# Performance work log

Measured on AMD Instinct MI355X. Metric: run time of the kernel, lower is better.

The kernel has to match this reference:

```python
import jax, jax.numpy as jnp
import numpy as np
from math import comb

LEVEL = 16
LENGTH = 64
TOPK = 2
SIZE = 512
BATCH = 32
NEG = -1e8


def _catalan(n_leaves):
    # number of distinct binary trees over n_leaves leaves
    m = n_leaves - 1
    return comb(2 * m, m) // (m + 1)


def _offsets(length, level):
    # cell offset of each chart level: level l occupies (length - l) cells
    return np.cumsum([0] + [length - l for l in range(level)])


def setup_inputs() -> dict:
    key = jax.random.key(0)
    K, B, size, level, length = TOPK, BATCH, SIZE, LEVEL, LENGTH
    L, N = length - level, level
    off = _offsets(length, level)
    ncells = int(off[-1])
    ks = jax.random.split(key, 5)
    chart_h = jax.random.normal(ks[0], (K, B, ncells, size), jnp.float32)
    chart_s = jax.random.normal(ks[1], (K, B, ncells, 1), jnp.float32)
    mat = jax.random.normal(ks[2], (size, size), jnp.float32) / np.sqrt(size).astype(np.float32)
    Wc = jax.random.normal(ks[3], (2 * size, size), jnp.float32) / np.sqrt(2 * size).astype(np.float32)
    bc = jnp.zeros((size,), jnp.float32)
    # structural gather indices: left child = (level n, pos), right child = (level level-1-n, pos+n+1)
    l_idx = np.zeros((L, N), np.int64)
    r_idx = np.zeros((L, N), np.int64)
    for pos in range(L):
        for n in range(N):
            l_idx[pos, n] = off[n] + pos
            r_idx[pos, n] = off[level - 1 - n] + pos + n + 1
    return {
        'chart_h': chart_h, 'chart_s': chart_s,
        'l_index': jnp.asarray(l_idx.reshape(-1)), 'r_index': jnp.asarray(r_idx.reshape(-1)),
        'mat': mat, 'Wc': Wc, 'bc': bc,
    }


def _penalty_mask(level, N, K):
    # Faithful to penalize_incomplete_splits: idx = i // K**2 == 0 for i < K*K,
    # so only the n_idx==0 block is ever penalized. l_level=0, r_level=level-1.
    M = N * K * K
    mask = np.zeros(M, bool)
    for i in range(K * K):
        lk, rk = i // K, i % K
        if _catalan(0 + 1) < lk + 1 or _catalan((level - 1) + 1) < rk + 1:
            mask[i] = True
    return jnp.asarray(mask)


def reference(chart_h, chart_s, l_index, r_index, mat, Wc, bc):
    K, B, ncells, size = chart_h.shape
    level = LEVEL
    N = level
    L = l_index.shape[0] // N
    M = N * K * K
    # gather child states from charts: (K,B,L,N,size) -> (B,L,N,K,size)
    lh = jnp.moveaxis(chart_h[:, :, l_index].reshape(K, B, L, N, size), 0, 3)
    rh = jnp.moveaxis(chart_h[:, :, r_index].reshape(K, B, L, N, size), 0, 3)
    ls = jnp.moveaxis(chart_s[:, :, l_index].reshape(K, B, L, N), 0, 3)  # (B,L,N,K)
    rs = jnp.moveaxis(chart_s[:, :, r_index].reshape(K, B, L, N), 0, 3)
    # bilinear composition score: (B,L,N,K_l,K_r)
    s_raw = jnp.einsum('blnkd,de,blnje->blnkj', lh, mat, rh)
    # flat combo index = n*K*K + lk*K + rk; add child scores
    s = (s_raw + ls[..., :, None] + rs[..., None, :]).reshape(B, L, M)
    s = jnp.where(_penalty_mask(level, N, K), jnp.float32(NEG), s)
    topk_s, topk_idx = jax.lax.top_k(s, K)  # (B,L,K), sorted descending like torch.topk
    # dense compose over all N*K*K combos
    combo_lh = jnp.repeat(lh, K, axis=3).reshape(B, L, M, size)   # lk = z // K
    combo_rh = jnp.tile(rh, (1, 1, 1, K, 1)).reshape(B, L, M, size)  # rk = z % K
    all_h = jnp.tanh(jnp.concatenate([combo_lh, combo_rh], axis=-1) @ Wc + bc)
    topk_h = jnp.take_along_axis(all_h, topk_idx[..., None], axis=2)  # (B,L,K,size)
    # UnitNorm normalize_func
    topk_h = topk_h / jnp.linalg.norm(topk_h, axis=-1, keepdims=True)
    topk_s = topk_s[..., None]  # (B,L,K,1) to match torch shape
    if _catalan(N + 1) < K:  # static no-op at this level
        topk_s = topk_s.at[:, :, _catalan(N + 1):].set(NEG)
    topk_n_idx = topk_idx // (K * K)
    topk_lk = (topk_idx % (K * K)) // K
    topk_rk = (topk_idx % (K * K)) % K
    return topk_h, topk_s, topk_n_idx, topk_lk, topk_rk
```

## Files before the change

kernel.cpp:

```cpp
#include <hip/hip_runtime.h>
#include <cstdint>
#include <cstddef>

#define B_DIM   32
#define L_DIM   48
#define NCELLS  904
#define SZ      512
#define NEGF    (-1e8f)
#define DELTA   0.25f
#define MAXC    32

#define OFF_S   1572864
#define OFF_N   1575936
#define OFF_L   1579008
#define OFF_R   1582080

typedef _Float16  f16x8 __attribute__((ext_vector_type(8)));
typedef float     f32x4 __attribute__((ext_vector_type(4)));

static __device__ __forceinline__ uint16_t f2bf(float f) {
    uint32_t u = __builtin_bit_cast(uint32_t, f);
    u += 0x7fffu + ((u >> 16) & 1u);
    return (uint16_t)(u >> 16);
}

#define GLD16(gp, lp) __builtin_amdgcn_global_load_lds(                        \
        (__attribute__((address_space(1))) void*)(gp),                         \
        (__attribute__((address_space(3))) void*)(lp), 16, 0, 0)

static __device__ __forceinline__ int level_off(int n) {
    return n * 64 - (n * (n - 1)) / 2;
}

__global__ __launch_bounds__(256)
void prep_mat(const float* __restrict__ mat, _Float16* __restrict__ P)
{
    const int tg   = blockIdx.x * 256 + threadIdx.x;
    const int c    = tg >> 6, lane = tg & 63;
    const int srow = 16 * (c & 31) + (lane & 15);
    const int scol = 32 * (c >> 5) + (lane >> 4) * 8;
    const float4 a = *(const float4*)(mat + (size_t)srow * 512 + scol);
    const float4 b = *(const float4*)(mat + (size_t)srow * 512 + scol + 4);
    f16x8 w;
    w[0]=(_Float16)(a.x*64.f); w[1]=(_Float16)(a.y*64.f);
    w[2]=(_Float16)(a.z*64.f); w[3]=(_Float16)(a.w*64.f);
    w[4]=(_Float16)(b.x*64.f); w[5]=(_Float16)(b.y*64.f);
    w[6]=(_Float16)(b.z*64.f); w[7]=(_Float16)(b.w*64.f);
    *(f16x8*)(P + (size_t)tg * 8) = w;
}

__global__ __launch_bounds__(256)
void conv_h(const float* __restrict__ x, _Float16* __restrict__ y)
{
    const size_t i = ((size_t)blockIdx.x * 256 + threadIdx.x) * 8;
    const float4 a = *(const float4*)(x + i);
    const float4 b = *(const float4*)(x + i + 4);
    f16x8 w;
    w[0]=(_Float16)(a.x*16.f); w[1]=(_Float16)(a.y*16.f);
    w[2]=(_Float16)(a.z*16.f); w[3]=(_Float16)(a.w*16.f);
    w[4]=(_Float16)(b.x*16.f); w[5]=(_Float16)(b.y*16.f);
    w[6]=(_Float16)(b.z*16.f); w[7]=(_Float16)(b.w*16.f);
    *(f16x8*)(y + i) = w;
}

__global__ __launch_bounds__(256, 2)
void gemm_fused(const _Float16* __restrict__ A16,
                const _Float16* __restrict__ P,
                _Float16* __restrict__ C)
{
    __shared__ _Float16 As16[64 * 512];

    const int t = threadIdx.x;
    const int wave = t >> 6, lane = t & 63;
    const int n0 = blockIdx.x * 256;
    const int nq = n0 >> 4;
    const int m0 = blockIdx.y * 64;
    const int col_l = lane & 15, quad = lane >> 4;

#pragma unroll
    for (int i = 0; i < 16; ++i) {
        const int r = wave * 16 + i;
        GLD16(A16 + (size_t)(m0 + r) * 512 + ((lane ^ (r & 7)) * 8),
              (char*)As16 + r * 1024);
    }
    __syncthreads();

    f32x4 acc[4][4];
#pragma unroll
    for (int i = 0; i < 4; ++i)
#pragma unroll
        for (int j = 0; j < 4; ++j) acc[i][j] = (f32x4){0.f, 0.f, 0.f, 0.f};

#pragma unroll 4
    for (int w16 = 0; w16 < 16; ++w16) {
        f16x8 af[4];
#pragma unroll
        for (int mi = 0; mi < 4; ++mi) {
            const int r = mi * 16 + col_l;
            const int u = w16 * 4 + quad;
            af[mi] = *(const f16x8*)&As16[r * 512 + (u ^ (r & 7)) * 8];
        }
#pragma unroll
        for (int ni = 0; ni < 4; ++ni) {
            const int c = w16 * 32 + nq + wave * 4 + ni;
            const f16x8 bf = *(const f16x8*)(P + (size_t)c * 512 + lane * 8);
#pragma unroll
            for (int mi = 0; mi < 4; ++mi)
                acc[mi][ni] = __builtin_amdgcn_mfma_f32_16x16x32_f16(
                    af[mi], bf, acc[mi][ni], 0, 0, 0);
        }
    }

#pragma unroll
    for (int ni = 0; ni < 4; ++ni) {
        const int ncol = n0 + wave * 64 + ni * 16 + col_l;
#pragma unroll
        for (int mi = 0; mi < 4; ++mi) {
            const int mrow = m0 + mi * 16 + quad * 4;
#pragma unroll
            for (int r = 0; r < 4; ++r)
                C[(size_t)(mrow + r) * 512 + ncol] = (_Float16)acc[mi][ni][r];
        }
    }
}

static __device__ __forceinline__ void emit_outputs(
    int row, int i1, int i2, float v1, float v2, float* out)
{
    out[OFF_S + row * 2 + 0] = v1;
    out[OFF_S + row * 2 + 1] = v2;
    out[OFF_N + row * 2 + 0] = (float)(i1 >> 2);
    out[OFF_N + row * 2 + 1] = (float)(i2 >> 2);
    out[OFF_L + row * 2 + 0] = (float)((i1 >> 1) & 1);
    out[OFF_L + row * 2 + 1] = (float)((i2 >> 1) & 1);
    out[OFF_R + row * 2 + 0] = (float)(i1 & 1);
    out[OFF_R + row * 2 + 1] = (float)(i2 & 1);
}

static __device__ __forceinline__ void gather_x(
    int row, int pos, int b, const int* top_z,
    const float* __restrict__ chart_h, uint16_t* __restrict__ X, int tid)
{
#pragma unroll
    for (int kq = 0; kq < 2; ++kq) {
        const int z = top_z[kq];
        const int n = z >> 2, lk = (z >> 1) & 1, rk = z & 1;
        const int lcell = level_off(n) + pos;
        const int rcell = level_off(15 - n) + pos + n + 1;
        const float* srcl = chart_h + ((size_t)(lk * B_DIM + b) * NCELLS + lcell) * SZ;
        const float* srcr = chart_h + ((size_t)(rk * B_DIM + b) * NCELLS + rcell) * SZ;
        uint16_t* dst = X + ((size_t)row * 2 + kq) * 1024;
        const int e = tid * 2;
        const float2 a = *(const float2*)(srcl + e);
        const float2 c = *(const float2*)(srcr + e);
        *(uint32_t*)(dst + e)       = (uint32_t)f2bf(a.x) | ((uint32_t)f2bf(a.y) << 16);
        *(uint32_t*)(dst + 512 + e) = (uint32_t)f2bf(c.x) | ((uint32_t)f2bf(c.y) << 16);
    }
}

__global__ __launch_bounds__(256)
void score_topk(const float* __restrict__ chart_h,
                const _Float16* __restrict__ CH16,
                const _Float16* __restrict__ T16,
                const float* __restrict__ chart_s,
                uint32_t* __restrict__ items,
                int* __restrict__ rowbase,
                int* __restrict__ counter,
                int* __restrict__ flags,
                uint16_t* __restrict__ X,
                float* __restrict__ out)
{
    const int b   = blockIdx.x / L_DIM;
    const int pos = blockIdx.x % L_DIM;
    const int row = blockIdx.x;
    const int wave = threadIdx.x >> 6, lane = threadIdx.x & 63;

    __shared__ float s_sh[64];
    __shared__ int top_z[2];
    __shared__ int flag_sh;

#pragma unroll
    for (int ni = 0; ni < 4; ++ni) {
        const int n = wave * 4 + ni;
        const int lcell = level_off(n) + pos;
        const int rcell = level_off(15 - n) + pos + n + 1;

        const f16x8 lv0 = *(const f16x8*)(CH16 + ((size_t)(0 * B_DIM + b) * NCELLS + lcell) * SZ + lane * 8);
        const f16x8 lv1 = *(const f16x8*)(CH16 + ((size_t)(1 * B_DIM + b) * NCELLS + lcell) * SZ + lane * 8);
        const f16x8 t0 = *(const f16x8*)(T16 + ((size_t)(0 * B_DIM + b) * NCELLS + rcell) * SZ + lane * 8);
        const f16x8 t1 = *(const f16x8*)(T16 + ((size_t)(1 * B_DIM + b) * NCELLS + rcell) * SZ + lane * 8);

        float d00 = 0.f, d01 = 0.f, d10 = 0.f, d11 = 0.f;
#pragma unroll
        for (int j = 0; j < 8; ++j) {
            const float c0 = (float)t0[j], c1 = (float)t1[j];
            const float l0 = (float)lv0[j], l1 = (float)lv1[j];
            d00 += l0 * c0; d01 += l0 * c1;
            d10 += l1 * c0; d11 += l1 * c1;
        }
#pragma unroll
        for (int o = 32; o > 0; o >>= 1) {
            d00 += __shfl_down(d00, o);
            d01 += __shfl_down(d01, o);
            d10 += __shfl_down(d10, o);
            d11 += __shfl_down(d11, o);
        }
        if (lane == 0) {
            const float ls0 = chart_s[(size_t)(0 * B_DIM + b) * NCELLS + lcell];
            const float ls1 = chart_s[(size_t)(1 * B_DIM + b) * NCELLS + lcell];
            const float rs0 = chart_s[(size_t)(0 * B_DIM + b) * NCELLS + rcell];
            const float rs1 = chart_s[(size_t)(1 * B_DIM + b) * NCELLS + rcell];
            const float inv = 1.0f / 16384.0f;
            s_sh[n * 4 + 0] = d00 * inv + ls0 + rs0;
            s_sh[n * 4 + 1] = d01 * inv + ls0 + rs1;
            s_sh[n * 4 + 2] = d10 * inv + ls1 + rs0;
            s_sh[n * 4 + 3] = d11 * inv + ls1 + rs1;
        }
    }
    __syncthreads();

    if (threadIdx.x < 64) {
        float v = s_sh[lane];
        if (lane == 2 || lane == 3) v = NEGF;
        float v1 = v; int i1 = lane;
#pragma unroll
        for (int o = 32; o > 0; o >>= 1) {
            float ov = __shfl_down(v1, o);
            int   oi = __shfl_down(i1, o);
            if (ov > v1 || (ov == v1 && oi < i1)) { v1 = ov; i1 = oi; }
        }
        v1 = __shfl(v1, 0); i1 = __shfl(i1, 0);
        float v2 = (lane == i1) ? -3.4e38f : v; int i2 = lane;
#pragma unroll
        for (int o = 32; o > 0; o >>= 1) {
            float ov = __shfl_down(v2, o);
            int   oi = __shfl_down(i2, o);
            if (ov > v2 || (ov == v2 && oi < i2)) { v2 = ov; i2 = oi; }
        }
        v2 = __shfl(v2, 0); i2 = __shfl(i2, 0);
        float v3 = (lane == i1 || lane == i2) ? -3.4e38f : v;
#pragma unroll
        for (int o = 32; o > 0; o >>= 1) {
            const float ov = __shfl_down(v3, o);
            if (ov > v3) v3 = ov;
        }
        v3 = __shfl(v3, 0);

        const int f = (v1 - v2 < DELTA) || (v2 - v3 < DELTA);
        const bool cand = (v >= v2 - DELTA);
        const unsigned long long mask = __ballot(cand);
        const int nc_full = __popcll(mask);
        const int nc = nc_full < MAXC ? nc_full : MAXC;
        int base = 0;
        if (lane == 0) {
            flags[row] = f ? nc : 0;
            flag_sh = f;
            if (f) base = atomicAdd(counter, nc);
            rowbase[row] = base;
            top_z[0] = i1; top_z[1] = i2;
            if (!f) emit_outputs(row, i1, i2, v1, v2, out);
        }
        base = __shfl(base, 0);
        if (f && cand) {
            const int rank = __popcll(mask & ((1ull << lane) - 1ull));
            if (rank < MAXC) items[base + rank] = ((uint32_t)row << 6) | (uint32_t)lane;
        }
    }
    __syncthreads();

    if (!flag_sh)
        gather_x(row, pos, b, top_z, chart_h, X, threadIdx.x);
}

__global__ __launch_bounds__(256)
void refine_eval(const float* __restrict__ chart_h,
                 const float* __restrict__ chart_s,
                 const float* __restrict__ mat,
                 const uint32_t* __restrict__ items,
                 const int* __restrict__ counter,
                 float* __restrict__ exval)
{
    const int total = *counter;
    const int t = threadIdx.x;
    const int wave = t >> 6, lane = t & 63;

    __shared__ float lh_sh[2][512];
    __shared__ float psum[2][4];

    for (int p = blockIdx.x; 2 * p < total; p += gridDim.x) {
        const int it0 = 2 * p;
        const int it1v = (2 * p + 1 < total);
        const uint32_t item0 = items[it0];
        const uint32_t item1 = it1v ? items[it0 + 1] : item0;

        int rowA = item0 >> 6, zA = item0 & 63;
        int bA = rowA / L_DIM, posA = rowA % L_DIM;
        int nA = zA >> 2, lkA = (zA >> 1) & 1, rkA = zA & 1;
        int lcA = level_off(nA) + posA, rcA = level_off(15 - nA) + posA + nA + 1;
        int rowB = item1 >> 6, zB = item1 & 63;
        int bB = rowB / L_DIM, posB = rowB % L_DIM;
        int nB = zB >> 2, lkB = (zB >> 1) & 1, rkB = zB & 1;
        int lcB = level_off(nB) + posB, rcB = level_off(15 - nB) + posB + nB + 1;

        const float* lhA = chart_h + ((size_t)(lkA * B_DIM + bA) * NCELLS + lcA) * SZ;
        const float* rhA = chart_h + ((size_t)(rkA * B_DIM + bA) * NCELLS + rcA) * SZ;
        const float* lhB = chart_h + ((size_t)(lkB * B_DIM + bB) * NCELLS + lcB) * SZ;
        const float* rhB = chart_h + ((size_t)(rkB * B_DIM + bB) * NCELLS + rcB) * SZ;

        __syncthreads();
        lh_sh[0][t] = lhA[t]; lh_sh[0][t + 256] = lhA[t + 256];
        lh_sh[1][t] = lhB[t]; lh_sh[1][t + 256] = lhB[t + 256];
        const float4 rA0 = *(const float4*)(rhA + lane * 8);
        const float4 rA1 = *(const float4*)(rhA + lane * 8 + 4);
        const float4 rB0 = *(const float4*)(rhB + lane * 8);
        const float4 rB1 = *(const float4*)(rhB + lane * 8 + 4);
        __syncthreads();

        const float* mb = mat + (size_t)(wave * 128) * 512 + lane * 8;
        float a00 = 0.f, a01 = 0.f, b00 = 0.f, b01 = 0.f;
        for (int e = 0; e < 128; e += 2) {
            const float4 m0 = *(const float4*)(mb + (size_t)(e + 0) * 512);
            const float4 m1 = *(const float4*)(mb + (size_t)(e + 0) * 512 + 4);
            const float4 m2 = *(const float4*)(mb + (size_t)(e + 1) * 512);
            const float4 m3 = *(const float4*)(mb + (size_t)(e + 1) * 512 + 4);
            const int eg = wave * 128 + e;
            const float lA0 = lh_sh[0][eg],     lB0 = lh_sh[1][eg];
            const float lA1 = lh_sh[0][eg + 1], lB1 = lh_sh[1][eg + 1];
            const float dA0 = m0.x*rA0.x + m0.y*rA0.y + m0.z*rA0.z + m0.w*rA0.w
                            + m1.x*rA1.x + m1.y*rA1.y + m1.z*rA1.z + m1.w*rA1.w;
            const float dB0 = m0.x*rB0.x + m0.y*rB0.y + m0.z*rB0.z + m0.w*rB0.w
                            + m1.x*rB1.x + m1.y*rB1.y + m1.z*rB1.z + m1.w*rB1.w;
            const float dA1 = m2.x*rA0.x + m2.y*rA0.y + m2.z*rA0.z + m2.w*rA0.w
                            + m3.x*rA1.x + m3.y*rA1.y + m3.z*rA1.z + m3.w*rA1.w;
            const float dB1 = m2.x*rB0.x + m2.y*rB0.y + m2.z*rB0.z + m2.w*rB0.w
                            + m3.x*rB1.x + m3.y*rB1.y + m3.z*rB1.z + m3.w*rB1.w;
            a00 += lA0 * dA0; a01 += lA1 * dA1;
            b00 += lB0 * dB0; b01 += lB1 * dB1;
        }
        float sA = a00 + a01, sB = b00 + b01;
#pragma unroll
        for (int o = 32; o > 0; o >>= 1) {
            sA += __shfl_down(sA, o);
            sB += __shfl_down(sB, o);
        }
        if (lane == 0) { psum[0][wave] = sA; psum[1][wave] = sB; }
        __syncthreads();
        if (t == 0) {
            const float lsA = chart_s[(size_t)(lkA * B_DIM + bA) * NCELLS + lcA];
            const float rsA = chart_s[(size_t)(rkA * B_DIM + bA) * NCELLS + rcA];
            exval[it0] = psum[0][0] + psum[0][1] + psum[0][2] + psum[0][3] + lsA + rsA;
            if (it1v) {
                const float lsB = chart_s[(size_t)(lkB * B_DIM + bB) * NCELLS + lcB];
                const float rsB = chart_s[(size_t)(rkB * B_DIM + bB) * NCELLS + rcB];
                exval[it0 + 1] = psum[1][0] + psum[1][1] + psum[1][2] + psum[1][3] + lsB + rsB;
            }
        }
    }
}

__global__ __launch_bounds__(256)
void refine_pick(const float* __restrict__ chart_h,
                 const uint32_t* __restrict__ items,
                 const int* __restrict__ rowbase,
                 const int* __restrict__ flags,
                 const float* __restrict__ exval,
                 uint16_t* __restrict__ X,
                 float* __restrict__ out)
{
    const int row = blockIdx.x;
    const int nc = flags[row];
    if (nc == 0) return;
    const int b = row / L_DIM, pos = row % L_DIM;
    const int t = threadIdx.x;

    __shared__ int top_z[2];

    if (t == 0) {
        const int base = rowbase[row];
        float v1 = -3.4e38f; int c1 = -1;
        for (int c = 0; c < nc; ++c) {
            const float v = exval[base + c];
            if (v > v1) { v1 = v; c1 = c; }
        }
        float v2 = -3.4e38f; int c2 = -1;
        for (int c = 0; c < nc; ++c) {
            if (c == c1) continue;
            const float v = exval[base + c];
            if (v > v2) { v2 = v; c2 = c; }
        }
        const int i1 = (int)(items[base + c1] & 63u);
        const int i2 = (int)(items[base + c2] & 63u);
        top_z[0] = i1; top_z[1] = i2;
        emit_outputs(row, i1, i2, v1, v2, out);
    }
    __syncthreads();
    gather_x(row, pos, b, top_z, chart_h, X, t);
}

__global__ __launch_bounds__(256)
void transpose_wc(const float* __restrict__ Wc, uint16_t* __restrict__ WcT)
{
    __shared__ float tbuf[64][65];
    const int i0 = blockIdx.x * 64;
    const int o0 = blockIdx.y * 64;
    const int c = threadIdx.x & 63, r4 = threadIdx.x >> 6;
    for (int rr = r4; rr < 64; rr += 4)
        tbuf[rr][c] = Wc[(size_t)(i0 + rr) * 512 + o0 + c];
    __syncthreads();
    for (int rr = r4; rr < 64; rr += 4)
        WcT[(size_t)(o0 + rr) * 1024 + i0 + c] = f2bf(tbuf[c][rr]);
}

typedef __bf16 bf16x8 __attribute__((ext_vector_type(8)));

__global__ __launch_bounds__(256, 2)
void gemm_compose(const uint16_t* __restrict__ A,
                  const uint16_t* __restrict__ Bm,
                  const float* __restrict__ bias,
                  float* __restrict__ C,
                  int M, int Nn, int Kk)
{
    __shared__ uint16_t As[128 * 64];
    __shared__ uint16_t Bs[128 * 64];

    const int tid  = threadIdx.x;
    const int wave = tid >> 6, lane = tid & 63;
    const int m0 = blockIdx.x * 128, n0 = blockIdx.y * 128;
    const int wm = (wave & 1) * 64, wn = (wave >> 1) * 64;
    const int col_l = lane & 15, quad = lane >> 4;
    const int lrow = lane >> 3;
    const int lcol = (lane & 7) * 8;

    f32x4 acc[4][4];
#pragma unroll
    for (int i = 0; i < 4; ++i)
#pragma unroll
        for (int j = 0; j < 4; ++j) acc[i][j] = (f32x4){0.f, 0.f, 0.f, 0.f};

    for (int k0 = 0; k0 < Kk; k0 += 64) {
        __syncthreads();
#pragma unroll
        for (int i = 0; i < 4; ++i) {
            const int q = wave * 4 + i;
            const int r = q * 8 + lrow;
            GLD16(A  + (size_t)(m0 + r) * Kk + k0 + lcol, (char*)As + q * 1024);
            GLD16(Bm + (size_t)(n0 + r) * Kk + k0 + lcol, (char*)Bs + q * 1024);
        }
        __syncthreads();
#pragma unroll
        for (int kk = 0; kk < 64; kk += 32) {
            bf16x8 af[4], bfr[4];
#pragma unroll
            for (int mi = 0; mi < 4; ++mi)
                af[mi] = *(const bf16x8*)&As[(wm + mi * 16 + col_l) * 64 + kk + quad * 8];
#pragma unroll
            for (int ni = 0; ni < 4; ++ni)
                bfr[ni] = *(const bf16x8*)&Bs[(wn + ni * 16 + col_l) * 64 + kk + quad * 8];
#pragma unroll
            for (int mi = 0; mi < 4; ++mi)
#pragma unroll
                for (int ni = 0; ni < 4; ++ni)
                    acc[mi][ni] = __builtin_amdgcn_mfma_f32_16x16x32_bf16(
                        af[mi], bfr[ni], acc[mi][ni], 0, 0, 0);
        }
    }

#pragma unroll
    for (int ni = 0; ni < 4; ++ni) {
        const int ncol = n0 + wn + ni * 16 + col_l;
        const float bv = bias[ncol];
#pragma unroll
        for (int mi = 0; mi < 4; ++mi) {
            const int mrow = m0 + wm + mi * 16 + quad * 4;
#pragma unroll
            for (int r = 0; r < 4; ++r)
                C[(size_t)(mrow + r) * Nn + ncol] = tanhf(acc[mi][ni][r] + bv);
        }
    }
}

__global__ __launch_bounds__(256)
void norm_rows(const float* __restrict__ H, float* __restrict__ out)
{
    const int row = blockIdx.x;
    const float* h = H + (size_t)row * SZ;
    const int t = threadIdx.x;
    const int wave = t >> 6, lane = t & 63;
    const float a = h[t], c = h[t + 256];
    float ss = a * a + c * c;
#pragma unroll
    for (int o = 32; o > 0; o >>= 1) ss += __shfl_down(ss, o);
    __shared__ float wsum[4];
    if (lane == 0) wsum[wave] = ss;
    __syncthreads();
    const float inv = rsqrtf(wsum[0] + wsum[1] + wsum[2] + wsum[3]);
    out[(size_t)row * SZ + t]       = a * inv;
    out[(size_t)row * SZ + t + 256] = c * inv;
}

extern "C" void kernel_launch(void* const* d_in, const int* in_sizes, int n_in,
                              void* d_out, int out_size, void* d_ws, size_t ws_size,
                              hipStream_t stream)
{
    const float* chart_h = (const float*)d_in[0];
    const float* chart_s = (const float*)d_in[1];
    const float* mat = (const float*)d_in[4];
    const float* Wc  = (const float*)d_in[5];
    const float* bc  = (const float*)d_in[6];
    float* out = (float*)d_out;

    char* ws = (char*)d_ws;
    _Float16* T16   = (_Float16*)ws;
    _Float16* MAT16 = (_Float16*)(ws + 59244544);
    uint32_t* ITEMS = (uint32_t*)(ws + 59768832);
    float*    EXVAL = (float*)(ws + 59965440);
    int*      RBASE = (int*)(ws + 60162048);
    int*      CNT   = (int*)(ws + 60168192);
    int*      FLAGS = (int*)(ws + 60168448);
    uint16_t* X     = (uint16_t*)(ws + 60174592);
    _Float16* CH16  = (_Float16*)(ws + 66466048);
    uint16_t* WcT   = (uint16_t*)ws;
    float*    H     = (float*)(ws + 1048576);

    hipMemsetAsync(CNT, 0, 4, stream);
    prep_mat<<<dim3(128), 256, 0, stream>>>(mat, MAT16);
    conv_h<<<dim3(14464), 256, 0, stream>>>(chart_h, CH16);
    gemm_fused<<<dim3(2, 904), 256, 0, stream>>>(CH16, MAT16, T16);
    score_topk<<<dim3(B_DIM * L_DIM), 256, 0, stream>>>(chart_h, CH16, T16, chart_s,
                                                        ITEMS, RBASE, CNT, FLAGS, X, out);
    transpose_wc<<<dim3(16, 8), 256, 0, stream>>>(Wc, WcT);
    refine_eval<<<dim3(1024), 256, 0, stream>>>(chart_h, chart_s, mat, ITEMS, CNT, EXVAL);
    refine_pick<<<dim3(B_DIM * L_DIM), 256, 0, stream>>>(chart_h, ITEMS, RBASE, FLAGS,
                                                         EXVAL, X, out);
    gemm_compose<<<dim3(24, 4), 256, 0, stream>>>(X, WcT, bc, H, 3072, 512, 1024);
    norm_rows<<<dim3(3072), 256, 0, stream>>>(H, out);
}
```

Baseline: 341.6 us.

## Fuse mat-projection GEMM into score kernel, computing only needed right-child rows

The standalone GEMM that projected every chart cell through mat and wrote a large fp16 T buffer to global memory is removed. Each score block now loads its 32 right-child rows (16 splits × 2 k) into shared memory, multiplies them by the fp16 mat with MFMA, and keeps the result in shared memory for the dot products. This removes the round trip of the T buffer through global memory and skips projecting cells that are never used as right children. In exchange, every block rereads the whole fp16 mat from cache and needs more shared memory per block. conv_h also now converts 16 elements per thread, and the workspace layout is compacted so CH16 and WcT share space.

```diff
diff --git a/kernel.cpp b/kernel.cpp
--- a/kernel.cpp
+++ b/kernel.cpp
@@ -52,75 +52,17 @@
 __global__ __launch_bounds__(256)
 void conv_h(const float* __restrict__ x, _Float16* __restrict__ y)
 {
-    const size_t i = ((size_t)blockIdx.x * 256 + threadIdx.x) * 8;
-    const float4 a = *(const float4*)(x + i);
-    const float4 b = *(const float4*)(x + i + 4);
-    f16x8 w;
-    w[0]=(_Float16)(a.x*16.f); w[1]=(_Float16)(a.y*16.f);
-    w[2]=(_Float16)(a.z*16.f); w[3]=(_Float16)(a.w*16.f);
-    w[4]=(_Float16)(b.x*16.f); w[5]=(_Float16)(b.y*16.f);
-    w[6]=(_Float16)(b.z*16.f); w[7]=(_Float16)(b.w*16.f);
-    *(f16x8*)(y + i) = w;
-}
-
-__global__ __launch_bounds__(256, 2)
-void gemm_fused(const _Float16* __restrict__ A16,
-                const _Float16* __restrict__ P,
-                _Float16* __restrict__ C)
-{
-    __shared__ _Float16 As16[64 * 512];
-
-    const int t = threadIdx.x;
-    const int wave = t >> 6, lane = t & 63;
-    const int n0 = blockIdx.x * 256;
-    const int nq = n0 >> 4;
-    const int m0 = blockIdx.y * 64;
-    const int col_l = lane & 15, quad = lane >> 4;
-
-#pragma unroll
-    for (int i = 0; i < 16; ++i) {
-        const int r = wave * 16 + i;
-        GLD16(A16 + (size_t)(m0 + r) * 512 + ((lane ^ (r & 7)) * 8),
-              (char*)As16 + r * 1024);
-    }
-    __syncthreads();
-
-    f32x4 acc[4][4];
-#pragma unroll
-    for (int i = 0; i < 4; ++i)
-#pragma unroll
-        for (int j = 0; j < 4; ++j) acc[i][j] = (f32x4){0.f, 0.f, 0.f, 0.f};
-
-#pragma unroll 4
-    for (int w16 = 0; w16 < 16; ++w16) {
-        f16x8 af[4];
-#pragma unroll
-        for (int mi = 0; mi < 4; ++mi) {
-            const int r = mi * 16 + col_l;
-            const int u = w16 * 4 + quad;
-            af[mi] = *(const f16x8*)&As16[r * 512 + (u ^ (r & 7)) * 8];
-        }
-#pragma unroll
-        for (int ni = 0; ni < 4; ++ni) {
-            const int c = w16 * 32 + nq + wave * 4 + ni;
-            const f16x8 bf = *(const f16x8*)(P + (size_t)c * 512 + lane * 8);
-#pragma unroll
-            for (int mi = 0; mi < 4; ++mi)
-                acc[mi][ni] = __builtin_amdgcn_mfma_f32_16x16x32_f16(
-                    af[mi], bf, acc[mi][ni], 0, 0, 0);
-        }
-    }
-
-#pragma unroll
-    for (int ni = 0; ni < 4; ++ni) {
-        const int ncol = n0 + wave * 64 + ni * 16 + col_l;
-#pragma unroll
-        for (int mi = 0; mi < 4; ++mi) {
-            const int mrow = m0 + mi * 16 + quad * 4;
-#pragma unroll
-            for (int r = 0; r < 4; ++r)
-                C[(size_t)(mrow + r) * 512 + ncol] = (_Float16)acc[mi][ni][r];
-        }
+    const size_t i = ((size_t)blockIdx.x * 256 + threadIdx.x) * 16;
+#pragma unroll
+    for (int h = 0; h < 2; ++h) {
+        const float4 a = *(const float4*)(x + i + h * 8);
+        const float4 b = *(const float4*)(x + i + h * 8 + 4);
+        f16x8 w;
+        w[0]=(_Float16)(a.x*16.f); w[1]=(_Float16)(a.y*16.f);
+        w[2]=(_Float16)(a.z*16.f); w[3]=(_Float16)(a.w*16.f);
+        w[4]=(_Float16)(b.x*16.f); w[5]=(_Float16)(b.y*16.f);
+        w[6]=(_Float16)(b.z*16.f); w[7]=(_Float16)(b.w*16.f);
+        *(f16x8*)(y + i + h * 8) = w;
     }
 }
 
@@ -158,26 +100,77 @@
     }
 }
 
-__global__ __launch_bounds__(256)
-void score_topk(const float* __restrict__ chart_h,
-                const _Float16* __restrict__ CH16,
-                const _Float16* __restrict__ T16,
-                const float* __restrict__ chart_s,
-                uint32_t* __restrict__ items,
-                int* __restrict__ rowbase,
-                int* __restrict__ counter,
-                int* __restrict__ flags,
-                uint16_t* __restrict__ X,
-                float* __restrict__ out)
-{
-    const int b   = blockIdx.x / L_DIM;
-    const int pos = blockIdx.x % L_DIM;
-    const int row = blockIdx.x;
-    const int wave = threadIdx.x >> 6, lane = threadIdx.x & 63;
-
+__global__ __launch_bounds__(256, 2)
+void score_fused(const float* __restrict__ chart_h,
+                 const _Float16* __restrict__ CH16,
+                 const _Float16* __restrict__ P,
+                 const float* __restrict__ chart_s,
+                 uint32_t* __restrict__ items,
+                 int* __restrict__ rowbase,
+                 int* __restrict__ counter,
+                 int* __restrict__ flags,
+                 uint16_t* __restrict__ X,
+                 float* __restrict__ out)
+{
+    __shared__ _Float16 Arh[32 * 512];
+    __shared__ _Float16 Ts[32 * 512];
     __shared__ float s_sh[64];
     __shared__ int top_z[2];
     __shared__ int flag_sh;
+
+    const int row = blockIdx.x;
+    const int b   = row / L_DIM;
+    const int pos = row % L_DIM;
+    const int t = threadIdx.x;
+    const int wave = t >> 6, lane = t & 63;
+    const int col_l = lane & 15, quad = lane >> 4;
+
+#pragma unroll
+    for (int i = 0; i < 8; ++i) {
+        const int r = wave * 8 + i;
+        const int k = r >> 4, n = r & 15;
+        const int rcell = level_off(15 - n) + pos + n + 1;
+        const size_t grow = (size_t)(k * B_DIM + b) * NCELLS + rcell;
+        GLD16(CH16 + grow * 512 + ((lane ^ (r & 7)) * 8),
+              (char*)Arh + r * 1024);
+    }
+    __syncthreads();
+
+    f32x4 acc[2][8];
+#pragma unroll
+    for (int i = 0; i < 2; ++i)
+#pragma unroll
+        for (int j = 0; j < 8; ++j) acc[i][j] = (f32x4){0.f, 0.f, 0.f, 0.f};
+
+#pragma unroll 4
+    for (int w16 = 0; w16 < 16; ++w16) {
+        f16x8 af[2];
+#pragma unroll
+        for (int mi = 0; mi < 2; ++mi) {
+            const int r = mi * 16 + col_l;
+            const int u = w16 * 4 + quad;
+            af[mi] = *(const f16x8*)&Arh[r * 512 + (u ^ (r & 7)) * 8];
+        }
+#pragma unroll
+        for (int ni = 0; ni < 8; ++ni) {
+            const int c = w16 * 32 + wave * 8 + ni;
+            const f16x8 bf = *(const f16x8*)(P + (size_t)c * 512 + lane * 8);
+#pragma unroll
+            for (int mi = 0; mi < 2; ++mi)
+                acc[mi][ni] = __builtin_amdgcn_mfma_f32_16x16x32_f16(
+                    af[mi], bf, acc[mi][ni], 0, 0, 0);
+        }
+    }
+
+#pragma unroll
+    for (int mi = 0; mi < 2; ++mi)
+#pragma unroll
+        for (int ni = 0; ni < 8; ++ni)
+#pragma unroll
+            for (int rr = 0; rr < 4; ++rr)
+                Ts[(mi * 16 + quad * 4 + rr) * 512 + wave * 128 + ni * 16 + col_l]
+                    = (_Float16)acc[mi][ni][rr];
+    __syncthreads();
 
 #pragma unroll
     for (int ni = 0; ni < 4; ++ni) {
@@ -187,8 +180,8 @@
 
         const f16x8 lv0 = *(const f16x8*)(CH16 + ((size_t)(0 * B_DIM + b) * NCELLS + lcell) * SZ + lane * 8);
         const f16x8 lv1 = *(const f16x8*)(CH16 + ((size_t)(1 * B_DIM + b) * NCELLS + lcell) * SZ + lane * 8);
-        const f16x8 t0 = *(const f16x8*)(T16 + ((size_t)(0 * B_DIM + b) * NCELLS + rcell) * SZ + lane * 8);
-        const f16x8 t1 = *(const f16x8*)(T16 + ((size_t)(1 * B_DIM + b) * NCELLS + rcell) * SZ + lane * 8);
+        const f16x8 t0 = *(const f16x8*)&Ts[(0 * 16 + n) * 512 + lane * 8];
+        const f16x8 t1 = *(const f16x8*)&Ts[(1 * 16 + n) * 512 + lane * 8];
 
         float d00 = 0.f, d01 = 0.f, d10 = 0.f, d11 = 0.f;
 #pragma unroll
@@ -510,24 +503,23 @@
     float* out = (float*)d_out;
 
     char* ws = (char*)d_ws;
-    _Float16* T16   = (_Float16*)ws;
-    _Float16* MAT16 = (_Float16*)(ws + 59244544);
-    uint32_t* ITEMS = (uint32_t*)(ws + 59768832);
-    float*    EXVAL = (float*)(ws + 59965440);
-    int*      RBASE = (int*)(ws + 60162048);
-    int*      CNT   = (int*)(ws + 60168192);
-    int*      FLAGS = (int*)(ws + 60168448);
-    uint16_t* X     = (uint16_t*)(ws + 60174592);
-    _Float16* CH16  = (_Float16*)(ws + 66466048);
-    uint16_t* WcT   = (uint16_t*)ws;
-    float*    H     = (float*)(ws + 1048576);
+    _Float16* MAT16 = (_Float16*)ws;
+    uint32_t* ITEMS = (uint32_t*)(ws + 524288);
+    float*    EXVAL = (float*)(ws + 720896);
+    int*      RBASE = (int*)(ws + 917504);
+    int*      CNT   = (int*)(ws + 923648);
+    int*      FLAGS = (int*)(ws + 923904);
+    uint16_t* X     = (uint16_t*)(ws + 930048);
+    _Float16* CH16  = (_Float16*)(ws + 7221504);
+    uint16_t* WcT   = (uint16_t*)(ws + 7221504);
+    float*    H     = (float*)(ws + 8270080);
 
     hipMemsetAsync(CNT, 0, 4, stream);
     prep_mat<<<dim3(128), 256, 0, stream>>>(mat, MAT16);
-    conv_h<<<dim3(14464), 256, 0, stream>>>(chart_h, CH16);
-    gemm_fused<<<dim3(2, 904), 256, 0, stream>>>(CH16, MAT16, T16);
-    score_topk<<<dim3(B_DIM * L_DIM), 256, 0, stream>>>(chart_h, CH16, T16, chart_s,
-                                                        ITEMS, RBASE, CNT, FLAGS, X, out);
+    conv_h<<<dim3(7232), 256, 0, stream>>>(chart_h, CH16);
+    score_fused<<<dim3(B_DIM * L_DIM), 256, 0, stream>>>(chart_h, CH16, MAT16,
+                                                         chart_s, ITEMS, RBASE,
+                                                         CNT, FLAGS, X, out);
     transpose_wc<<<dim3(16, 8), 256, 0, stream>>>(Wc, WcT);
     refine_eval<<<dim3(1024), 256, 0, stream>>>(chart_h, chart_s, mat, ITEMS, CNT, EXVAL);
     refine_pick<<<dim3(B_DIM * L_DIM), 256, 0, stream>>>(chart_h, ITEMS, RBASE, FLAGS,
```

After: 346.3 us. No clear change (+1.4%).
